# Optimization experiments

Measured on AMD Instinct MI355X. Metric: run time of the kernel, lower is better.

The kernel has to match this reference:

```python
import jax, jax.numpy as jnp
import numpy as np

COMBS = ((0, 1), (0, 2), (1, 2))
OUT_DIM, TIME_RANK, RANK = 3, 4, 4


def grid_sample_nd(grid, coords):
    """Multilinear interpolation. grid: [C, *R] (d spatial dims), coords: [N, d] in [-1, 1].
    align_corners=True, border clamp. Returns [N, C]."""
    d = coords.shape[-1]
    i0s, ws = [], []
    for k in range(d):
        R = grid.shape[1 + k]
        x = jnp.clip((coords[:, k] + 1.0) * 0.5 * (R - 1), 0.0, R - 1)
        i0 = jnp.clip(jnp.floor(x).astype(jnp.int32), 0, R - 2)
        i0s.append(i0)
        ws.append(x - i0)
    out = jnp.zeros((grid.shape[0], coords.shape[0]), grid.dtype)
    for corner in range(2 ** d):
        idx, w = [], jnp.ones((coords.shape[0],), grid.dtype)
        for k in range(d):
            b = (corner >> k) & 1
            idx.append(i0s[k] + b)
            w = w * (ws[k] if b else 1.0 - ws[k])
        out = out + grid[(slice(None),) + tuple(idx)] * w  # [C, N]
    return out.T


def setup_inputs():
    key = jax.random.key(0)
    ks = jax.random.split(key, 16)
    n_rays, S = 4096, 128
    N = n_rays * S
    R, T, F = 128, 150, 32
    rays_d = jax.random.normal(ks[0], (n_rays, 3), jnp.float32)
    pts = jax.random.uniform(ks[1], (N, 3), jnp.float32, -1.0, 1.0)
    times = jax.random.uniform(ks[2], (N,), jnp.float32, -1.0, 1.0)
    deltas = jax.random.uniform(ks[3], (N,), jnp.float32) * 0.02 + 1e-3
    ridx = jnp.repeat(jnp.arange(n_rays, dtype=jnp.int32), S)
    boundary = (jnp.arange(N) % S) == 0
    bg_color = jax.random.uniform(ks[4], (n_rays, 3), jnp.float32)
    grid_space = jax.random.normal(ks[5], (3, RANK * OUT_DIM * TIME_RANK, R, R), jnp.float32) * 0.1
    grid_time = jax.random.normal(ks[6], (OUT_DIM * TIME_RANK, T), jnp.float32) * 0.1
    features = jax.random.normal(ks[7], (F, R, R, R), jnp.float32) * 0.1
    W1 = jax.random.normal(ks[8], (F + 3, 64), jnp.float32) * 0.05
    b1 = jnp.zeros((64,), jnp.float32)
    W2 = jax.random.normal(ks[9], (64, 16), jnp.float32) * 0.05
    b2 = jnp.zeros((16,), jnp.float32)
    Wc1 = jax.random.normal(ks[10], (15 + 3, 64), jnp.float32) * 0.05
    bc1 = jnp.zeros((64,), jnp.float32)
    Wc2 = jax.random.normal(ks[11], (64, 3), jnp.float32) * 0.05
    bc2 = jnp.zeros((3,), jnp.float32)
    return {"rays_d": rays_d, "pts": pts, "times": times, "deltas": deltas,
            "bg_color": bg_color, "grid_space": grid_space, "grid_time": grid_time,
            "features": features, "W1": W1, "b1": b1, "W2": W2, "b2": b2,
            "Wc1": Wc1, "bc1": bc1, "Wc2": Wc2, "bc2": bc2,
            "ridx": ridx, "boundary": boundary}


def reference(rays_d, pts, times, deltas, bg_color, grid_space, grid_time, features,
              W1, b1, W2, b2, Wc1, bc1, Wc2, bc2, ridx, boundary):
    n_rays = rays_d.shape[0]
    N = pts.shape[0]
    rays_d = rays_d / jnp.linalg.norm(rays_d, axis=-1, keepdims=True)
    rd = rays_d[ridx]  # [N, 3] per-sample ray dirs

    # --- low-rank spatio-temporal feature coordinates ---
    it = grid_sample_nd(grid_time, times[:, None]).reshape(N, OUT_DIM, TIME_RANK)
    sp = jnp.stack([grid_sample_nd(grid_space[c], pts[:, list(comb)])
                    for c, comb in enumerate(COMBS)])  # [3, N, rank*out*tr]
    sp = sp.reshape(3, N, OUT_DIM, TIME_RANK, RANK)
    sp = jnp.prod(sp, axis=0).sum(axis=-1)            # [N, out_dim, time_rank]
    coords = jnp.clip((sp * it).sum(axis=-1), -1.0, 1.0)  # [N, 3]
    feats = grid_sample_nd(features, coords)          # [N, F]

    # --- MLP decoder (sigma + color) ---
    h = jax.nn.relu(jnp.concatenate([feats, rd], axis=-1) @ W1 + b1)
    s = h @ W2 + b2
    sigma = jnp.exp(jnp.clip(s[:, 0], -15.0, 15.0))   # trunc_exp
    geo = s[:, 1:]
    hc = jax.nn.relu(jnp.concatenate([geo, rd], axis=-1) @ Wc1 + bc1)
    rgb = jax.nn.sigmoid(hc @ Wc2 + bc2)              # [N, 3]

    # --- segment volumetric integration (exclusive transmittance) ---
    tau = sigma * deltas
    excl = jnp.cumsum(tau) - tau
    bmask = boundary.astype(tau.dtype)
    seg_first = jax.ops.segment_sum(excl * bmask, ridx, num_segments=n_rays)
    Tr = jnp.exp(-(excl - seg_first[ridx]))
    w = Tr * (1.0 - jnp.exp(-tau))                    # per-sample weights
    ray_colors = jax.ops.segment_sum(w[:, None] * rgb, ridx, num_segments=n_rays)
    alpha = jax.ops.segment_sum(w, ridx, num_segments=n_rays)
    return ray_colors + (1.0 - alpha)[:, None] * bg_color
```

## Files before the change

kernel.cpp:

```cpp
#include <hip/hip_runtime.h>
#include <hip/hip_fp16.h>
#include <math.h>

#define RR 128
#define TT 150
#define NCH 48
#define NF 32

typedef float vf2 __attribute__((ext_vector_type(2)));
typedef unsigned int u4v __attribute__((ext_vector_type(4)));
typedef _Float16 h2 __attribute__((ext_vector_type(2)));
typedef _Float16 h4 __attribute__((ext_vector_type(4)));
typedef float fv4 __attribute__((ext_vector_type(4)));

__device__ __forceinline__ void up4(uint u, float s, float* a) {
    vf2 lo = __builtin_amdgcn_cvt_pk_f32_fp8(u, false);
    vf2 hi = __builtin_amdgcn_cvt_pk_f32_fp8(u, true);
    a[0] = fmaf(s, lo[0], a[0]); a[1] = fmaf(s, lo[1], a[1]);
    a[2] = fmaf(s, hi[0], a[2]); a[3] = fmaf(s, hi[1], a[3]);
}
__device__ __forceinline__ void up16(u4v q, float s, float* a) {
    up4(q[0], s, a + 0); up4(q[1], s, a + 4);
    up4(q[2], s, a + 8); up4(q[3], s, a + 12);
}
__device__ __forceinline__ float dot2(h2 a, h2 b, float c) {
    return __builtin_amdgcn_fdot2(a, b, c, false);
}
__device__ __forceinline__ h2 pack2(float a, float b) {
    h2 r; r[0] = (_Float16)a; r[1] = (_Float16)b; return r;
}
__device__ __forceinline__ h2 ash2(uint u) { return __builtin_bit_cast(h2, u); }

__global__ __launch_bounds__(256) void tgsp_8(const float* __restrict__ in,
                                              uint* __restrict__ out) {
    __shared__ float lds[48][65];
    const int t = threadIdx.x;
    const int p = blockIdx.x >> 8;
    const int tile = blockIdx.x & 255;
    const size_t V = (size_t)RR * RR;
    const size_t v0 = (size_t)tile * 64;
    const float* ip = in + (size_t)p * NCH * V;
    uint* op = out + (size_t)p * V * 12;
    #pragma unroll
    for (int k = 0; k < 12; k++) {
        int idx = k * 256 + t; int c = idx >> 6; int vv = idx & 63;
        lds[c][vv] = ip[(size_t)c * V + v0 + vv];
    }
    __syncthreads();
    #pragma unroll
    for (int k = 0; k < 3; k++) {
        int idx = k * 256 + t; int vv = idx / 12; int cp = idx - vv * 12;
        float a = lds[4 * cp + 0][vv] * 128.f;
        float b = lds[4 * cp + 1][vv] * 128.f;
        float c = lds[4 * cp + 2][vv] * 128.f;
        float d = lds[4 * cp + 3][vv] * 128.f;
        uint w = (uint)__builtin_amdgcn_cvt_pk_fp8_f32(a, b, 0, false);
        w = (uint)__builtin_amdgcn_cvt_pk_fp8_f32(c, d, w, true);
        op[(v0 + vv) * 12 + cp] = w;
    }
}

template<bool TR>
__global__ __launch_bounds__(256, 4) void lrv_main(
    const float* __restrict__ rays_d,
    const float* __restrict__ pts,
    const float* __restrict__ times,
    const float* __restrict__ deltas,
    const float* __restrict__ bg,
    const void* __restrict__ gspace_p,
    const float* __restrict__ gtime,
    const float* __restrict__ feat,
    const float* __restrict__ W1, const float* __restrict__ b1,
    const float* __restrict__ W2, const float* __restrict__ b2,
    const float* __restrict__ Wc1, const float* __restrict__ bc1,
    const float* __restrict__ Wc2, const float* __restrict__ bc2,
    const int*  __restrict__ ridx,
    float* __restrict__ out)
{
    __shared__ __align__(16) _Float16 sW1t[64 * 48];
    __shared__ __align__(16) _Float16 sW2t[16 * 72];
    __shared__ __align__(16) _Float16 sX[4 * 64 * 48];
    __shared__ __align__(16) h2 sWc1d[9 * 64];
    __shared__ __align__(16) h2 sWc2d[32 * 3];
    __shared__ float sb1[64], sbc1[64], sb2[16], sbc2[4];
    __shared__ __align__(16) float4 sFeatV[8][8];
    __shared__ int sV[4], sU[4];
    __shared__ float waveTot[4];
    __shared__ float4 rbuf[4];

    const int tid  = threadIdx.x;
    const int lane = tid & 63;
    const int wv   = tid >> 6;
    const int lg   = lane >> 4;
    const int ll   = lane & 15;

    {
        for (int k = tid; k < 64 * 48; k += 256) {
            int n = k / 48, kk = k - n * 48;
            sW1t[k] = (_Float16)((kk < 35) ? W1[kk * 64 + n] : 0.f);
        }
        for (int k = tid; k < 16 * 64; k += 256) {
            int o = k >> 6, n = k & 63;
            sW2t[o * 72 + n] = (_Float16)W2[n * 16 + o];
        }
        for (int k = tid; k < 9 * 64; k += 256) {
            int ip = k >> 6, j = k & 63;
            sWc1d[k] = pack2(Wc1[(2 * ip) * 64 + j], Wc1[(2 * ip + 1) * 64 + j]);
        }
        for (int k = tid; k < 32 * 3; k += 256) {
            int jp = k / 3, c = k - jp * 3;
            sWc2d[k] = pack2(Wc2[(2 * jp) * 3 + c], Wc2[(2 * jp + 1) * 3 + c]);
        }
        if (tid < 64) { sb1[tid] = b1[tid]; sbc1[tid] = bc1[tid]; }
        if (tid < 16) sb2[tid] = b2[tid];
        if (tid < 3)  sbc2[tid] = bc2[tid];
    }
    __syncthreads();

    const int ray = blockIdx.x * 2 + (tid >> 7);
    const int i   = ray * 128 + (tid & 127);

    float itv[12];
    {
        float t = times[i];
        float x = (t + 1.f) * 0.5f * (float)(TT - 1);
        x = fminf(fmaxf(x, 0.f), (float)(TT - 1));
        int ti0 = (int)floorf(x);
        ti0 = min(max(ti0, 0), TT - 2);
        float tw = x - (float)ti0;
        #pragma unroll
        for (int c = 0; c < 12; c++) {
            float v0 = gtime[c * TT + ti0];
            float v1 = gtime[c * TT + ti0 + 1];
            itv[c] = fmaf(tw, v1 - v0, v0);
        }
    }

    float p0 = pts[i * 3 + 0], p1 = pts[i * 3 + 1], p2 = pts[i * 3 + 2];
    int   pbia[3], pbib[3];
    float pw[3][4];
    {
        const float pa[3] = { p0, p0, p1 };
        const float pb[3] = { p1, p2, p2 };
        #pragma unroll
        for (int c = 0; c < 3; c++) {
            float xa = fminf(fmaxf((pa[c] + 1.f) * 0.5f * (float)(RR - 1), 0.f), (float)(RR - 1));
            float xb = fminf(fmaxf((pb[c] + 1.f) * 0.5f * (float)(RR - 1), 0.f), (float)(RR - 1));
            int ia = min(max((int)floorf(xa), 0), RR - 2);
            int ib = min(max((int)floorf(xb), 0), RR - 2);
            float wa = xa - (float)ia, wb = xb - (float)ib;
            pbia[c] = ia; pbib[c] = ib;
            pw[c][0] = (1.f - wa) * (1.f - wb);
            pw[c][1] = (1.f - wa) * wb;
            pw[c][2] = wa * (1.f - wb);
            pw[c][3] = wa * wb;
        }
    }
    float S12[12];
    if constexpr (TR) {
        const uint* gs = (const uint*)gspace_p;
        uint b[3][4];
        #pragma unroll
        for (int c = 0; c < 3; c++) {
            uint b00 = ((uint)c * (RR * RR) + (uint)pbia[c] * RR + (uint)pbib[c]) * 12u;
            b[c][0] = b00;            b[c][1] = b00 + 12u;
            b[c][2] = b00 + RR * 12u; b[c][3] = b00 + RR * 12u + 12u;
        }
        #pragma unroll
        for (int cb = 0; cb < 3; cb++) {
            float pr[16];
            #pragma unroll
            for (int p = 0; p < 3; p++) {
                float a[16];
                #pragma unroll
                for (int j = 0; j < 16; j++) a[j] = 0.f;
                #pragma unroll
                for (int corner = 0; corner < 4; corner++) {
                    u4v q = *reinterpret_cast<const u4v*>(gs + b[p][corner] + cb * 4);
                    up16(q, pw[p][corner] * 0.0078125f, a);
                }
                #pragma unroll
                for (int j = 0; j < 16; j++) pr[j] = (p == 0) ? a[j] : pr[j] * a[j];
            }
            #pragma unroll
            for (int g = 0; g < 4; g++)
                S12[cb * 4 + g] = pr[g * 4 + 0] + pr[g * 4 + 1]
                                + pr[g * 4 + 2] + pr[g * 4 + 3];
        }
    } else {
        const float* gs = (const float*)gspace_p;
        #pragma unroll
        for (int k = 0; k < 12; k++) S12[k] = 0.f;
        #pragma unroll 4
        for (int ch = 0; ch < NCH; ch++) {
            float prod = 1.f;
            #pragma unroll
            for (int c = 0; c < 3; c++) {
                const float* g = gs + (size_t)(c * NCH + ch) * (RR * RR)
                               + pbia[c] * RR + pbib[c];
                float v = pw[c][0] * g[0] + pw[c][1] * g[1]
                        + pw[c][2] * g[RR] + pw[c][3] * g[RR + 1];
                prod *= v;
            }
            S12[ch >> 2] += prod;
        }
    }
    float cc[3];
    #pragma unroll
    for (int o = 0; o < 3; o++) {
        float a = 0.f;
        #pragma unroll
        for (int t = 0; t < 4; t++) a += S12[o * 4 + t] * itv[o * 4 + t];
        cc[o] = fminf(fmaxf(a, -1.f), 1.f);
    }

    __align__(16) float in35[36];
    int   fi[3];
    float cw[8];
    {
        float fw[3];
        #pragma unroll
        for (int k = 0; k < 3; k++) {
            float xk = fminf(fmaxf((cc[k] + 1.f) * 0.5f * (float)(RR - 1), 0.f), (float)(RR - 1));
            int ik = min(max((int)floorf(xk), 0), RR - 2);
            fi[k] = ik; fw[k] = xk - (float)ik;
        }
        float w0 = fw[0], w1 = fw[1], w2 = fw[2];
        cw[0] = (1.f - w0) * (1.f - w1) * (1.f - w2);
        cw[1] = (1.f - w0) * (1.f - w1) * w2;
        cw[2] = (1.f - w0) * w1 * (1.f - w2);
        cw[3] = (1.f - w0) * w1 * w2;
        cw[4] = w0 * (1.f - w1) * (1.f - w2);
        cw[5] = w0 * (1.f - w1) * w2;
        cw[6] = w0 * w1 * (1.f - w2);
        cw[7] = w0 * w1 * w2;
    }
    {
        int packed = (fi[0] << 16) | (fi[1] << 8) | fi[2];
        int first  = __builtin_amdgcn_readfirstlane(packed);
        unsigned long long bal = __ballot(packed == first);
        if (lane == 0) { sV[wv] = first; sU[wv] = (bal == ~0ull) ? 1 : 0; }
    }
    __syncthreads();
    const bool uni = sU[0] && sU[1] && sU[2] && sU[3] &&
                     sV[0] == sV[1] && sV[1] == sV[2] && sV[2] == sV[3];
    const size_t V3 = (size_t)RR * RR * RR;
    if (uni) {
        {
            int c  = tid >> 5;
            int ch = tid & 31;
            size_t off = (((size_t)(fi[0] + ((c >> 2) & 1)) * RR
                         + (size_t)(fi[1] + ((c >> 1) & 1))) * RR
                         + (size_t)(fi[2] + (c & 1)));
            ((float*)sFeatV)[c * 32 + ch] = feat[(size_t)ch * V3 + off];
        }
        __syncthreads();
        float4* in4 = reinterpret_cast<float4*>(in35);
        #pragma unroll
        for (int chq = 0; chq < 8; chq++) {
            float4 acc = make_float4(0.f, 0.f, 0.f, 0.f);
            #pragma unroll
            for (int c = 0; c < 8; c++) {
                float4 v = sFeatV[c][chq];
                acc.x = fmaf(cw[c], v.x, acc.x);
                acc.y = fmaf(cw[c], v.y, acc.y);
                acc.z = fmaf(cw[c], v.z, acc.z);
                acc.w = fmaf(cw[c], v.w, acc.w);
            }
            in4[chq] = acc;
        }
    } else {
        size_t fb = ((size_t)fi[0] * RR + fi[1]) * RR + fi[2];
        #pragma unroll 4
        for (int ch = 0; ch < NF; ch++) {
            const float* f = feat + (size_t)ch * V3 + fb;
            in35[ch] = cw[0] * f[0]            + cw[1] * f[1]
                     + cw[2] * f[RR]           + cw[3] * f[RR + 1]
                     + cw[4] * f[RR * RR]      + cw[5] * f[RR * RR + 1]
                     + cw[6] * f[RR * RR + RR] + cw[7] * f[RR * RR + RR + 1];
        }
    }
    {
        int r = ridx[i];
        float d0 = rays_d[r * 3 + 0], d1 = rays_d[r * 3 + 1], d2 = rays_d[r * 3 + 2];
        float inv = 1.f / sqrtf(d0 * d0 + d1 * d1 + d2 * d2);
        in35[32] = d0 * inv; in35[33] = d1 * inv; in35[34] = d2 * inv;
    }

    _Float16* Xw = sX + wv * (64 * 48);
    float* Srow  = (float*)Xw;

    {
        u4v xw[6];
        #pragma unroll
        for (int t6 = 0; t6 < 6; t6++) {
            #pragma unroll
            for (int e = 0; e < 4; e++) {
                int q = t6 * 4 + e;
                float a = (2 * q     < 35) ? in35[2 * q]     : 0.f;
                float b = (2 * q + 1 < 35) ? in35[2 * q + 1] : 0.f;
                xw[t6][e] = __builtin_bit_cast(uint, pack2(a, b));
            }
        }
        u4v* xrow = (u4v*)(Xw + lane * 48);
        #pragma unroll
        for (int t6 = 0; t6 < 6; t6++) xrow[t6] = xw[t6];
    }

    fv4 bb[4];
    #pragma unroll
    for (int hr = 0; hr < 4; hr++)
        bb[hr] = *(const fv4*)&sb1[hr * 16 + (lg << 2)];
    fv4 b2v = *(const fv4*)&sb2[lg << 2];

    #pragma unroll
    for (int half = 0; half < 2; half++) {
        fv4 acc1[4][2];
        #pragma unroll
        for (int hr = 0; hr < 4; hr++) {
            acc1[hr][0] = bb[hr];
            acc1[hr][1] = bb[hr];
        }
        #pragma unroll
        for (int ks = 0; ks < 3; ks++) {
            h4 a1[4], b1f[2];
            #pragma unroll
            for (int hr = 0; hr < 4; hr++)
                a1[hr] = *(const h4*)&sW1t[(hr * 16 + ll) * 48 + ks * 16 + (lg << 2)];
            #pragma unroll
            for (int s2 = 0; s2 < 2; s2++) {
                int sc = half * 2 + s2;
                b1f[s2] = *(const h4*)&Xw[(sc * 16 + ll) * 48 + ks * 16 + (lg << 2)];
            }
            #pragma unroll
            for (int hr = 0; hr < 4; hr++) {
                acc1[hr][0] = __builtin_amdgcn_mfma_f32_16x16x16f16(a1[hr], b1f[0], acc1[hr][0], 0, 0, 0);
                acc1[hr][1] = __builtin_amdgcn_mfma_f32_16x16x16f16(a1[hr], b1f[1], acc1[hr][1], 0, 0, 0);
            }
        }
        #pragma unroll
        for (int s2 = 0; s2 < 2; s2++) {
            fv4 acc2 = b2v;
            #pragma unroll
            for (int ks = 0; ks < 4; ks++) {
                fv4 g = acc1[ks][s2];
                h4 hb;
                #pragma unroll
                for (int e = 0; e < 4; e++) hb[e] = (_Float16)fmaxf(g[e], 0.f);
                h4 a2 = *(const h4*)&sW2t[ll * 72 + ks * 16 + (lg << 2)];
                acc2 = __builtin_amdgcn_mfma_f32_16x16x16f16(a2, hb, acc2, 0, 0, 0);
            }
            int sc = half * 2 + s2;
            *(fv4*)&Srow[(sc * 16 + ll) * 20 + (lg << 2)] = acc2;
        }
    }

    float sacc[16];
    #pragma unroll
    for (int q = 0; q < 4; q++) {
        fv4 v = *(const fv4*)&Srow[lane * 20 + q * 4];
        sacc[q * 4 + 0] = v[0]; sacc[q * 4 + 1] = v[1];
        sacc[q * 4 + 2] = v[2]; sacc[q * 4 + 3] = v[3];
    }
    float sigma = expf(fminf(fmaxf(sacc[0], -15.f), 15.f));

    h2 xc[9];
    #pragma unroll
    for (int p = 0; p < 7; p++) xc[p] = pack2(sacc[2 * p + 1], sacc[2 * p + 2]);
    xc[7] = pack2(sacc[15], in35[32]);
    xc[8] = pack2(in35[33], in35[34]);

    float rc0 = sbc2[0], rc1 = sbc2[1], rc2 = sbc2[2];
    #pragma unroll 2
    for (int jb = 0; jb < 16; jb++) {
        float a0 = sbc1[jb * 4 + 0], a1 = sbc1[jb * 4 + 1];
        float a2 = sbc1[jb * 4 + 2], a3 = sbc1[jb * 4 + 3];
        #pragma unroll
        for (int p = 0; p < 9; p++) {
            u4v u = *reinterpret_cast<const u4v*>(&sWc1d[p * 64 + jb * 4]);
            h2 xp = xc[p];
            a0 = dot2(xp, ash2(u[0]), a0);
            a1 = dot2(xp, ash2(u[1]), a1);
            a2 = dot2(xp, ash2(u[2]), a2);
            a3 = dot2(xp, ash2(u[3]), a3);
        }
        a0 = fmaxf(a0, 0.f); a1 = fmaxf(a1, 0.f);
        a2 = fmaxf(a2, 0.f); a3 = fmaxf(a3, 0.f);
        h2 h01 = pack2(a0, a1), h23 = pack2(a2, a3);
        int jp0 = 2 * jb, jp1 = 2 * jb + 1;
        rc0 = dot2(h01, sWc2d[jp0 * 3 + 0], dot2(h23, sWc2d[jp1 * 3 + 0], rc0));
        rc1 = dot2(h01, sWc2d[jp0 * 3 + 1], dot2(h23, sWc2d[jp1 * 3 + 1], rc1));
        rc2 = dot2(h01, sWc2d[jp0 * 3 + 2], dot2(h23, sWc2d[jp1 * 3 + 2], rc2));
    }
    float r_ = 1.f / (1.f + expf(-rc0));
    float g_ = 1.f / (1.f + expf(-rc1));
    float b_ = 1.f / (1.f + expf(-rc2));

    float tau = sigma * deltas[i];
    float v = tau;
    #pragma unroll
    for (int off = 1; off < 64; off <<= 1) {
        float u = __shfl_up(v, off, 64);
        if (lane >= off) v += u;
    }
    if (lane == 63) waveTot[wv] = v;
    float excl = v - tau;
    __syncthreads();
    if (wv & 1) excl += waveTot[wv & 2];

    float Tr = expf(-excl);
    float w  = Tr * (1.f - expf(-tau));

    float ax = w * r_, ay = w * g_, az = w * b_, aw = w;
    #pragma unroll
    for (int off = 32; off; off >>= 1) {
        ax += __shfl_down(ax, off, 64);
        ay += __shfl_down(ay, off, 64);
        az += __shfl_down(az, off, 64);
        aw += __shfl_down(aw, off, 64);
    }
    if (lane == 0) rbuf[wv] = make_float4(ax, ay, az, aw);
    __syncthreads();
    if (lane == 0 && (wv & 1) == 0) {
        float cx = rbuf[wv].x + rbuf[wv + 1].x;
        float cy = rbuf[wv].y + rbuf[wv + 1].y;
        float cz = rbuf[wv].z + rbuf[wv + 1].z;
        float alpha = rbuf[wv].w + rbuf[wv + 1].w;
        out[ray * 3 + 0] = cx + (1.f - alpha) * bg[ray * 3 + 0];
        out[ray * 3 + 1] = cy + (1.f - alpha) * bg[ray * 3 + 1];
        out[ray * 3 + 2] = cz + (1.f - alpha) * bg[ray * 3 + 2];
    }
}

extern "C" void kernel_launch(void* const* d_in, const int* in_sizes, int n_in,
                              void* d_out, int out_size, void* d_ws, size_t ws_size,
                              hipStream_t stream) {
    const float* rays_d = (const float*)d_in[0];
    const float* pts    = (const float*)d_in[1];
    const float* times  = (const float*)d_in[2];
    const float* deltas = (const float*)d_in[3];
    const float* bg     = (const float*)d_in[4];
    const float* gspace = (const float*)d_in[5];
    const float* gtime  = (const float*)d_in[6];
    const float* feat   = (const float*)d_in[7];
    const float* W1  = (const float*)d_in[8];
    const float* b1  = (const float*)d_in[9];
    const float* W2  = (const float*)d_in[10];
    const float* b2  = (const float*)d_in[11];
    const float* Wc1 = (const float*)d_in[12];
    const float* bc1 = (const float*)d_in[13];
    const float* Wc2 = (const float*)d_in[14];
    const float* bc2 = (const float*)d_in[15];
    const int*   ridx = (const int*)d_in[16];

    const int n_rays = in_sizes[0] / 3;

    const size_t GSP_8B = (size_t)3 * RR * RR * NCH;

    if (ws_size >= GSP_8B) {
        uint* gsp_t = (uint*)d_ws;
        tgsp_8<<<dim3(3 * 256), dim3(256), 0, stream>>>(gspace, gsp_t);
        lrv_main<true><<<dim3(n_rays / 2), dim3(256), 0, stream>>>(
            rays_d, pts, times, deltas, bg, (const void*)gsp_t, gtime, feat,
            W1, b1, W2, b2, Wc1, bc1, Wc2, bc2, ridx, (float*)d_out);
    } else {
        lrv_main<false><<<dim3(n_rays / 2), dim3(256), 0, stream>>>(
            rays_d, pts, times, deltas, bg, (const void*)gspace, gtime, feat,
            W1, b1, W2, b2, Wc1, bc1, Wc2, bc2, ridx, (float*)d_out);
    }
}
```

Before: 119.1 us.

## Move color MLP to MFMA, pack fp8 unpack math, alias LDS, use fast exp

The per-thread fdot2 color MLP (18->64->3) is replaced by MFMA 16x16x16 f16 tiles. Its inputs are staged through the per-wave sX buffer, and the results are gathered back to lanes with shuffles. The fp8 plane decode now uses packed float2 FMAs. sFeatV is aliased onto sX to save LDS, which needs an extra __syncthreads before sX is reused. expf calls become __expf. This cuts VALU instruction count in the color MLP and plane gather, at the cost of extra LDS traffic, one more barrier and slightly lower exp precision.

```diff
diff --git a/kernel.cpp b/kernel.cpp
--- a/kernel.cpp
+++ b/kernel.cpp
@@ -13,23 +13,18 @@
 typedef _Float16 h4 __attribute__((ext_vector_type(4)));
 typedef float fv4 __attribute__((ext_vector_type(4)));
 
-__device__ __forceinline__ void up4(uint u, float s, float* a) {
-    vf2 lo = __builtin_amdgcn_cvt_pk_f32_fp8(u, false);
-    vf2 hi = __builtin_amdgcn_cvt_pk_f32_fp8(u, true);
-    a[0] = fmaf(s, lo[0], a[0]); a[1] = fmaf(s, lo[1], a[1]);
-    a[2] = fmaf(s, hi[0], a[2]); a[3] = fmaf(s, hi[1], a[3]);
-}
-__device__ __forceinline__ void up16(u4v q, float s, float* a) {
-    up4(q[0], s, a + 0); up4(q[1], s, a + 4);
-    up4(q[2], s, a + 8); up4(q[3], s, a + 12);
-}
-__device__ __forceinline__ float dot2(h2 a, h2 b, float c) {
-    return __builtin_amdgcn_fdot2(a, b, c, false);
-}
 __device__ __forceinline__ h2 pack2(float a, float b) {
     h2 r; r[0] = (_Float16)a; r[1] = (_Float16)b; return r;
 }
-__device__ __forceinline__ h2 ash2(uint u) { return __builtin_bit_cast(h2, u); }
+__device__ __forceinline__ void up4p(uint u, vf2 s, vf2* a) {
+    a[0] += __builtin_amdgcn_cvt_pk_f32_fp8(u, false) * s;
+    a[1] += __builtin_amdgcn_cvt_pk_f32_fp8(u, true) * s;
+}
+__device__ __forceinline__ void up16p(u4v q, float sf, vf2* a) {
+    vf2 s; s[0] = sf; s[1] = sf;
+    up4p(q[0], s, a + 0); up4p(q[1], s, a + 2);
+    up4p(q[2], s, a + 4); up4p(q[3], s, a + 6);
+}
 
 __global__ __launch_bounds__(256) void tgsp_8(const float* __restrict__ in,
                                               uint* __restrict__ out) {
@@ -78,15 +73,15 @@
     float* __restrict__ out)
 {
     __shared__ __align__(16) _Float16 sW1t[64 * 48];
-    __shared__ __align__(16) _Float16 sW2t[16 * 72];
+    __shared__ __align__(16) _Float16 sW2t[16 * 68];
+    __shared__ __align__(16) _Float16 sWc1t[64 * 36];
+    __shared__ __align__(16) _Float16 sWc2t[16 * 68];
     __shared__ __align__(16) _Float16 sX[4 * 64 * 48];
-    __shared__ __align__(16) h2 sWc1d[9 * 64];
-    __shared__ __align__(16) h2 sWc2d[32 * 3];
     __shared__ float sb1[64], sbc1[64], sb2[16], sbc2[4];
-    __shared__ __align__(16) float4 sFeatV[8][8];
     __shared__ int sV[4], sU[4];
     __shared__ float waveTot[4];
     __shared__ float4 rbuf[4];
+    float4 (*sFeatV)[8] = reinterpret_cast<float4(*)[8]>(sX);
 
     const int tid  = threadIdx.x;
     const int lane = tid & 63;
@@ -99,17 +94,17 @@
             int n = k / 48, kk = k - n * 48;
             sW1t[k] = (_Float16)((kk < 35) ? W1[kk * 64 + n] : 0.f);
         }
-        for (int k = tid; k < 16 * 64; k += 256) {
-            int o = k >> 6, n = k & 63;
-            sW2t[o * 72 + n] = (_Float16)W2[n * 16 + o];
-        }
-        for (int k = tid; k < 9 * 64; k += 256) {
-            int ip = k >> 6, j = k & 63;
-            sWc1d[k] = pack2(Wc1[(2 * ip) * 64 + j], Wc1[(2 * ip + 1) * 64 + j]);
-        }
-        for (int k = tid; k < 32 * 3; k += 256) {
-            int jp = k / 3, c = k - jp * 3;
-            sWc2d[k] = pack2(Wc2[(2 * jp) * 3 + c], Wc2[(2 * jp + 1) * 3 + c]);
+        for (int k = tid; k < 16 * 68; k += 256) {
+            int o = k / 68, n = k - o * 68;
+            sW2t[k] = (_Float16)((n < 64) ? W2[n * 16 + o] : 0.f);
+        }
+        for (int k = tid; k < 64 * 36; k += 256) {
+            int n = k / 36, kk = k - n * 36;
+            sWc1t[k] = (_Float16)((kk < 18) ? Wc1[kk * 64 + n] : 0.f);
+        }
+        for (int k = tid; k < 16 * 68; k += 256) {
+            int o = k / 68, n = k - o * 68;
+            sWc2t[k] = (_Float16)((o < 3 && n < 64) ? Wc2[n * 3 + o] : 0.f);
         }
         if (tid < 64) { sb1[tid] = b1[tid]; sbc1[tid] = bc1[tid]; }
         if (tid < 16) sb2[tid] = b2[tid];
@@ -168,24 +163,24 @@
         }
         #pragma unroll
         for (int cb = 0; cb < 3; cb++) {
-            float pr[16];
+            vf2 pr[8];
             #pragma unroll
             for (int p = 0; p < 3; p++) {
-                float a[16];
+                vf2 a[8];
                 #pragma unroll
-                for (int j = 0; j < 16; j++) a[j] = 0.f;
+                for (int j = 0; j < 8; j++) { a[j][0] = 0.f; a[j][1] = 0.f; }
                 #pragma unroll
                 for (int corner = 0; corner < 4; corner++) {
                     u4v q = *reinterpret_cast<const u4v*>(gs + b[p][corner] + cb * 4);
-                    up16(q, pw[p][corner] * 0.0078125f, a);
+                    up16p(q, pw[p][corner] * 0.0078125f, a);
                 }
                 #pragma unroll
-                for (int j = 0; j < 16; j++) pr[j] = (p == 0) ? a[j] : pr[j] * a[j];
+                for (int j = 0; j < 8; j++) pr[j] = (p == 0) ? a[j] : pr[j] * a[j];
             }
             #pragma unroll
             for (int g = 0; g < 4; g++)
-                S12[cb * 4 + g] = pr[g * 4 + 0] + pr[g * 4 + 1]
-                                + pr[g * 4 + 2] + pr[g * 4 + 3];
+                S12[cb * 4 + g] = pr[2 * g][0] + pr[2 * g][1]
+                                + pr[2 * g + 1][0] + pr[2 * g + 1][1];
         }
     } else {
         const float* gs = (const float*)gspace_p;
@@ -286,6 +281,7 @@
         float inv = 1.f / sqrtf(d0 * d0 + d1 * d1 + d2 * d2);
         in35[32] = d0 * inv; in35[33] = d1 * inv; in35[34] = d2 * inv;
     }
+    __syncthreads();
 
     _Float16* Xw = sX + wv * (64 * 48);
     float* Srow  = (float*)Xw;
@@ -347,7 +343,7 @@
                 h4 hb;
                 #pragma unroll
                 for (int e = 0; e < 4; e++) hb[e] = (_Float16)fmaxf(g[e], 0.f);
-                h4 a2 = *(const h4*)&sW2t[ll * 72 + ks * 16 + (lg << 2)];
+                h4 a2 = *(const h4*)&sW2t[ll * 68 + ks * 16 + (lg << 2)];
                 acc2 = __builtin_amdgcn_mfma_f32_16x16x16f16(a2, hb, acc2, 0, 0, 0);
             }
             int sc = half * 2 + s2;
@@ -362,39 +358,70 @@
         sacc[q * 4 + 0] = v[0]; sacc[q * 4 + 1] = v[1];
         sacc[q * 4 + 2] = v[2]; sacc[q * 4 + 3] = v[3];
     }
-    float sigma = expf(fminf(fmaxf(sacc[0], -15.f), 15.f));
-
-    h2 xc[9];
-    #pragma unroll
-    for (int p = 0; p < 7; p++) xc[p] = pack2(sacc[2 * p + 1], sacc[2 * p + 2]);
-    xc[7] = pack2(sacc[15], in35[32]);
-    xc[8] = pack2(in35[33], in35[34]);
-
-    float rc0 = sbc2[0], rc1 = sbc2[1], rc2 = sbc2[2];
-    #pragma unroll 2
-    for (int jb = 0; jb < 16; jb++) {
-        float a0 = sbc1[jb * 4 + 0], a1 = sbc1[jb * 4 + 1];
-        float a2 = sbc1[jb * 4 + 2], a3 = sbc1[jb * 4 + 3];
-        #pragma unroll
-        for (int p = 0; p < 9; p++) {
-            u4v u = *reinterpret_cast<const u4v*>(&sWc1d[p * 64 + jb * 4]);
-            h2 xp = xc[p];
-            a0 = dot2(xp, ash2(u[0]), a0);
-            a1 = dot2(xp, ash2(u[1]), a1);
-            a2 = dot2(xp, ash2(u[2]), a2);
-            a3 = dot2(xp, ash2(u[3]), a3);
-        }
-        a0 = fmaxf(a0, 0.f); a1 = fmaxf(a1, 0.f);
-        a2 = fmaxf(a2, 0.f); a3 = fmaxf(a3, 0.f);
-        h2 h01 = pack2(a0, a1), h23 = pack2(a2, a3);
-        int jp0 = 2 * jb, jp1 = 2 * jb + 1;
-        rc0 = dot2(h01, sWc2d[jp0 * 3 + 0], dot2(h23, sWc2d[jp1 * 3 + 0], rc0));
-        rc1 = dot2(h01, sWc2d[jp0 * 3 + 1], dot2(h23, sWc2d[jp1 * 3 + 1], rc1));
-        rc2 = dot2(h01, sWc2d[jp0 * 3 + 2], dot2(h23, sWc2d[jp1 * 3 + 2], rc2));
-    }
-    float r_ = 1.f / (1.f + expf(-rc0));
-    float g_ = 1.f / (1.f + expf(-rc1));
-    float b_ = 1.f / (1.f + expf(-rc2));
+    float sigma = __expf(fminf(fmaxf(sacc[0], -15.f), 15.f));
+
+    {
+        float xi[18];
+        #pragma unroll
+        for (int k = 0; k < 15; k++) xi[k] = sacc[k + 1];
+        xi[15] = in35[32]; xi[16] = in35[33]; xi[17] = in35[34];
+        uint wd[16];
+        #pragma unroll
+        for (int q = 0; q < 9; q++)
+            wd[q] = __builtin_bit_cast(uint, pack2(xi[2 * q], (2 * q + 1 < 18) ? xi[2 * q + 1] : 0.f));
+        #pragma unroll
+        for (int q = 9; q < 16; q++) wd[q] = 0u;
+        u4v* xrow = (u4v*)(Xw + lane * 48);
+        #pragma unroll
+        for (int t4 = 0; t4 < 4; t4++) {
+            u4v v; v[0] = wd[t4 * 4 + 0]; v[1] = wd[t4 * 4 + 1];
+                   v[2] = wd[t4 * 4 + 2]; v[3] = wd[t4 * 4 + 3];
+            xrow[t4] = v;
+        }
+    }
+    fv4 bbc[4];
+    #pragma unroll
+    for (int hr = 0; hr < 4; hr++)
+        bbc[hr] = *(const fv4*)&sbc1[hr * 16 + (lg << 2)];
+    fv4 c2bias;
+    c2bias[0] = (lg == 0) ? sbc2[0] : 0.f;
+    c2bias[1] = (lg == 0) ? sbc2[1] : 0.f;
+    c2bias[2] = (lg == 0) ? sbc2[2] : 0.f;
+    c2bias[3] = 0.f;
+
+    float rc0 = 0.f, rc1 = 0.f, rc2 = 0.f;
+    #pragma unroll
+    for (int sc = 0; sc < 4; sc++) {
+        fv4 acc1c[4];
+        #pragma unroll
+        for (int hr = 0; hr < 4; hr++) acc1c[hr] = bbc[hr];
+        #pragma unroll
+        for (int ks = 0; ks < 2; ks++) {
+            h4 bfrag = *(const h4*)&Xw[(sc * 16 + ll) * 48 + ks * 16 + (lg << 2)];
+            #pragma unroll
+            for (int hr = 0; hr < 4; hr++) {
+                h4 a = *(const h4*)&sWc1t[(hr * 16 + ll) * 36 + ks * 16 + (lg << 2)];
+                acc1c[hr] = __builtin_amdgcn_mfma_f32_16x16x16f16(a, bfrag, acc1c[hr], 0, 0, 0);
+            }
+        }
+        fv4 acc2c = c2bias;
+        #pragma unroll
+        for (int ks = 0; ks < 4; ks++) {
+            fv4 g = acc1c[ks];
+            h4 hb;
+            #pragma unroll
+            for (int e = 0; e < 4; e++) hb[e] = (_Float16)fmaxf(g[e], 0.f);
+            h4 a2 = *(const h4*)&sWc2t[ll * 68 + ks * 16 + (lg << 2)];
+            acc2c = __builtin_amdgcn_mfma_f32_16x16x16f16(a2, hb, acc2c, 0, 0, 0);
+        }
+        float t0 = __shfl(acc2c[0], ll, 64);
+        float t1 = __shfl(acc2c[1], ll, 64);
+        float t2 = __shfl(acc2c[2], ll, 64);
+        if (lg == sc) { rc0 = t0; rc1 = t1; rc2 = t2; }
+    }
+    float r_ = 1.f / (1.f + __expf(-rc0));
+    float g_ = 1.f / (1.f + __expf(-rc1));
+    float b_ = 1.f / (1.f + __expf(-rc2));
 
     float tau = sigma * deltas[i];
     float v = tau;
@@ -408,8 +435,8 @@
     __syncthreads();
     if (wv & 1) excl += waveTot[wv & 2];
 
-    float Tr = expf(-excl);
-    float w  = Tr * (1.f - expf(-tau));
+    float Tr = __expf(-excl);
+    float w  = Tr * (1.f - __expf(-tau));
 
     float ax = w * r_, ay = w * g_, az = w * b_, aw = w;
     #pragma unroll
```

After: 115.3 us (median of 2 runs). 1.03x faster.
